# Kernel optimization log

Measured on AMD Instinct MI355X. Metric: run time of the kernel, lower is better.

Reference implementation:

```python
import jax, jax.numpy as jnp
import numpy as np

N = 1024      # total nodes in batch
H = 128       # node_dim == hid_dim
B = 128       # number of graphs
NPG = 8       # nodes per graph (<= MAX_NODES=9)
MAXN = 9
BT = 3        # bond_types
A = 3 * MAXN * MAXN  # action_space_length = 243


def setup_inputs() -> dict:
    key = jax.random.key(0)
    ks = jax.random.split(key, 8)
    node_features = jax.random.normal(ks[0], (N, H), jnp.float32) * 0.5
    seg = np.repeat(np.arange(B), NPG)  # contiguous graph membership (dgl batching)
    segment_ids = jnp.asarray(seg, jnp.int32)
    # len_vec[g, n] = 1 if node n belongs to graph g  ->  len_vec.T @ len_vec is the block-diagonal pair mask
    len_vec = jnp.asarray((seg[None, :] == np.arange(B)[:, None]).astype(np.float32))
    mask = jnp.zeros((B, A), jnp.float32)  # additive logit mask
    rng = np.random.default_rng(0)
    indexmask = jnp.asarray(np.argsort(rng.random((B, A)), axis=1).astype(np.int32))  # per-graph permutation of [0,243)
    batch_num_nodes = jnp.full((B,), NPG, jnp.int32)
    sc = lambda k, sh, fan: jax.random.normal(k, sh, jnp.float32) / np.sqrt(fan)
    W_fcv1 = sc(ks[1], (H, H // 2), H); b_fcv1 = jnp.zeros((H // 2,), jnp.float32)
    W_fcv2 = sc(ks[2], (H // 2, 1), H // 2); b_fcv2 = jnp.zeros((1,), jnp.float32)
    W_a2 = sc(ks[3], (2 * H, H), 2 * H); b_a2 = jnp.zeros((H,), jnp.float32)
    W_final = sc(ks[4], (H, BT), H); b_final = jnp.zeros((BT,), jnp.float32)
    return dict(node_features=node_features, len_vec=len_vec, mask=mask,
                W_fcv1=W_fcv1, b_fcv1=b_fcv1, W_fcv2=W_fcv2, b_fcv2=b_fcv2,
                W_a2=W_a2, b_a2=b_a2, W_final=W_final, b_final=b_final,
                indexmask=indexmask, segment_ids=segment_ids,
                batch_num_nodes=batch_num_nodes)


def reference(node_features, len_vec, mask, W_fcv1, b_fcv1, W_fcv2, b_fcv2,
              W_a2, b_a2, W_final, b_final, indexmask, segment_ids,
              batch_num_nodes):
    # --- value head: sum-pool per graph, relu(fcv1), fcv2 ---
    readout = jax.ops.segment_sum(node_features, segment_ids, num_segments=B)  # [B,H]
    readout = jax.nn.relu(readout @ W_fcv1 + b_fcv1) @ W_fcv2 + b_fcv2          # [B,1]

    # --- all-pairs features: cat([nf[i], nf[j]]) -> relu -> action_2 -> relu -> final ---
    # relu(cat(a,b)) = cat(relu(a),relu(b)); split W_a2 so we never materialize [N,N,2H]
    r = jax.nn.relu(node_features)          # [N,H]
    Ai = r @ W_a2[:H]                        # row-node (Y2) contribution  [N,H]
    Bj = r @ W_a2[H:]                        # col-node (X2) contribution  [N,H]
    hidden = jax.nn.relu(Ai[:, None, :] + Bj[None, :, :] + b_a2)   # [N,N,H]
    len_matrix = (len_vec.T @ len_vec)[..., None]                  # [N,N,1] block-diagonal 0/1
    scores = (jnp.einsum('ijh,hk->ijk', hidden, W_final) + b_final) * len_matrix  # [N,N,3]
    flat = scores.reshape(-1)

    # --- ragged per-graph gather of the nonzero (in-block) entries, padded to A=243 ---
    val = batch_num_nodes.astype(jnp.int32)          # [B]
    off = jnp.cumsum(val) - val                      # exclusive prefix (node offsets)
    s = jnp.arange(A, dtype=jnp.int32)[None, :]      # [1,A] slot index
    v = val[:, None]; o = off[:, None]
    i_loc = s // (v * BT)
    j_loc = (s % (v * BT)) // BT
    k = s % BT
    valid = s < v * v * BT                           # slots beyond val*val*3 are padding (-1 in torch code)
    flat_idx = ((o + i_loc) * N + (o + j_loc)) * BT + k
    flat_idx = jnp.clip(flat_idx, 0, N * N * BT - 1)
    gathered = jnp.where(valid, flat[flat_idx], jnp.float32(0.0))  # [B,A]

    # torch.index_select(final[idx], 0, indexmask[idx])
    fap = jnp.take_along_axis(gathered, indexmask.astype(jnp.int32), axis=1)
    probs = jax.nn.softmax(fap + mask, axis=1)
    return probs, readout
```

## Files before the change

### kernel.cpp

```cpp
#include <hip/hip_runtime.h>
#include <cfloat>

#define HH 128
#define BB 128
#define AA 243
#define MAXV 9

__device__ __forceinline__ float rl(float x, int l) {
    return __builtin_bit_cast(float, __builtin_amdgcn_readlane(__builtin_bit_cast(int, x), l));
}

__global__ __launch_bounds__(512) void apm_fused(
    const float* __restrict__ nf,
    const float* __restrict__ maskp,
    const float* __restrict__ W_fcv1,
    const float* __restrict__ b_fcv1,
    const float* __restrict__ W_fcv2,
    const float* __restrict__ b_fcv2,
    const float* __restrict__ W_a2,
    const float* __restrict__ b_a2,
    const float* __restrict__ W_final,
    const float* __restrict__ b_final,
    const int*   __restrict__ indexmask,
    const int*   __restrict__ bnn,
    float* __restrict__ probs_out,
    float* __restrict__ readout_out)
{
    const int b    = blockIdx.x;
    const int t    = threadIdx.x;
    const int lane = t & 63;
    const int w    = t >> 6;
    const int matB = w >> 2;
    const int hq   = w & 3;
    const int c0   = lane << 1;

    __shared__ float pS[2][4][MAXV][132];
    __shared__ float wfT[3][HH];
    __shared__ float sc[AA + 1];
    __shared__ float rdbuf[HH];
    __shared__ float rout[64];
    __shared__ float xred[16];

    int ov = 0;
    if (lane < b)      ov += bnn[lane];
    if (lane + 64 < b) ov += bnn[lane + 64];
    const int v = bnn[b];

    const float* Wb = W_a2 + matB * (HH * HH) + (hq * 32) * HH + c0;
    float2 wreg[32];
    #pragma unroll
    for (int h = 0; h < 32; ++h) wreg[h] = *(const float2*)(Wb + h * HH);

    float mk = 0.f, bfin = 0.f; int im = 0;
    if (t < AA) {
        im   = indexmask[b * AA + t];
        mk   = maskp[b * AA + t];
        bfin = b_final[t % 3];
    }
    if (t < 3 * HH) {
        int h = t / 3, k = t - 3 * h;
        wfT[k][h] = W_final[t];
    }

    #pragma unroll
    for (int o = 1; o < 64; o <<= 1) ov += __shfl_xor(ov, o, 64);
    const int off = ov;

    const int hbase = hq * 32 + (lane & 31);
    float rr[MAXV]; float rdsum = 0.f;
    #pragma unroll
    for (int i = 0; i < MAXV; ++i) {
        float x = (i < v) ? nf[(off + i) * HH + hbase] : 0.f;
        rdsum += x;
        rr[i]  = fmaxf(x, 0.f);
    }
    if (w < 4 && lane < 32) rdbuf[hbase] = rdsum;

    float accx[MAXV], accy[MAXV];
    #pragma unroll
    for (int i = 0; i < MAXV; ++i) { accx[i] = 0.f; accy[i] = 0.f; }
    #pragma unroll
    for (int h = 0; h < 32; ++h) {
        const float wx = wreg[h].x, wy = wreg[h].y;
        #pragma unroll
        for (int i = 0; i < MAXV; ++i) {
            const float s = rl(rr[i], h);
            accx[i] = fmaf(s, wx, accx[i]);
            accy[i] = fmaf(s, wy, accy[i]);
        }
    }
    #pragma unroll
    for (int i = 0; i < MAXV; ++i)
        *(float2*)&pS[matB][hq][i][c0] = make_float2(accx[i], accy[i]);
    __syncthreads();

    const int vv3 = v * v * 3;
    if (t < AA && t >= vv3) sc[t] = 0.f;

    float a2lo = 0.f;
    if (w < 6) {
        #pragma unroll
        for (int rep = 0; rep < 3; ++rep) {
            int idx = t + rep * 384;
            int m   = idx / 576;
            int rem = idx - m * 576;
            int i   = rem >> 6;
            int cc  = (rem & 63) << 1;
            float2 p0 = *(const float2*)&pS[m][0][i][cc];
            float2 p1 = *(const float2*)&pS[m][1][i][cc];
            float2 p2 = *(const float2*)&pS[m][2][i][cc];
            float2 p3 = *(const float2*)&pS[m][3][i][cc];
            float sx = (p0.x + p1.x) + (p2.x + p3.x);
            float sy = (p0.y + p1.y) + (p2.y + p3.y);
            if (m == 0) { sx += b_a2[cc]; sy += b_a2[cc + 1]; }
            *(float2*)&pS[m][0][i][cc] = make_float2(sx, sy);
        }
    } else if (w == 6) {
        float rd1 = rdbuf[64 + lane];
        float q0 = 0.f, q1 = 0.f, q2 = 0.f, q3 = 0.f;
        #pragma unroll
        for (int h = 0; h < 16; ++h) {
            q0 = fmaf(rl(rd1, h),      W_fcv1[(64 + h)  * 64 + lane], q0);
            q1 = fmaf(rl(rd1, h + 16), W_fcv1[(80 + h)  * 64 + lane], q1);
            q2 = fmaf(rl(rd1, h + 32), W_fcv1[(96 + h)  * 64 + lane], q2);
            q3 = fmaf(rl(rd1, h + 48), W_fcv1[(112 + h) * 64 + lane], q3);
        }
        rout[lane] = (q0 + q1) + (q2 + q3);
    } else {
        float rd0 = rdbuf[lane];
        float q0 = b_fcv1[lane], q1 = 0.f, q2 = 0.f, q3 = 0.f;
        #pragma unroll
        for (int h = 0; h < 16; ++h) {
            q0 = fmaf(rl(rd0, h),      W_fcv1[h        * 64 + lane], q0);
            q1 = fmaf(rl(rd0, h + 16), W_fcv1[(16 + h) * 64 + lane], q1);
            q2 = fmaf(rl(rd0, h + 32), W_fcv1[(32 + h) * 64 + lane], q2);
            q3 = fmaf(rl(rd0, h + 48), W_fcv1[(48 + h) * 64 + lane], q3);
        }
        a2lo = (q0 + q1) + (q2 + q3);
    }
    __syncthreads();

    if (t < vv3) {
        const int pair = t / 3, k = t - 3 * pair;
        const int i = pair / v, j = pair - i * v;
        const float* ar = &pS[0][0][i][0];
        const float* br = &pS[1][0][j][0];
        const float* wk = &wfT[k][0];
        float s0 = 0.f, s1 = 0.f, s2 = 0.f, s3 = 0.f;
        #pragma unroll 8
        for (int h = 0; h < HH; h += 4) {
            float4 a4 = *(const float4*)(ar + h);
            float4 b4 = *(const float4*)(br + h);
            float4 w4 = *(const float4*)(wk + h);
            s0 = fmaf(fmaxf(a4.x + b4.x, 0.f), w4.x, s0);
            s1 = fmaf(fmaxf(a4.y + b4.y, 0.f), w4.y, s1);
            s2 = fmaf(fmaxf(a4.z + b4.z, 0.f), w4.z, s2);
            s3 = fmaf(fmaxf(a4.w + b4.w, 0.f), w4.w, s3);
        }
        sc[t] = bfin + ((s0 + s1) + (s2 + s3));
    } else if (w == 7) {
        float a2 = a2lo + rout[lane];
        float x = fmaxf(a2, 0.f) * W_fcv2[lane];
        #pragma unroll
        for (int o = 1; o < 64; o <<= 1) x += __shfl_xor(x, o, 64);
        if (lane == 0) readout_out[b] = x + b_fcv2[0];
    }
    __syncthreads();

    float x = -FLT_MAX;
    if (t < AA) x = sc[im] + mk;
    float m = x;
    #pragma unroll
    for (int o = 1; o < 64; o <<= 1) m = fmaxf(m, __shfl_xor(m, o, 64));
    if (lane == 0) xred[w] = m;
    __syncthreads();
    m = fmaxf(fmaxf(xred[0], xred[1]), fmaxf(xred[2], xred[3]));
    float e = (t < AA) ? __expf(x - m) : 0.f;
    float s = e;
    #pragma unroll
    for (int o = 1; o < 64; o <<= 1) s += __shfl_xor(s, o, 64);
    if (lane == 0) xred[8 + w] = s;
    __syncthreads();
    const float denom = (xred[8] + xred[9]) + (xred[10] + xred[11]);
    const float rden  = __builtin_amdgcn_rcpf(denom);
    if (t < AA) probs_out[b * AA + t] = e * rden;
}

extern "C" void kernel_launch(void* const* d_in, const int* in_sizes, int n_in,
                              void* d_out, int out_size, void* d_ws, size_t ws_size,
                              hipStream_t stream) {
    const float* nf      = (const float*)d_in[0];
    const float* maskp   = (const float*)d_in[2];
    const float* W_fcv1  = (const float*)d_in[3];
    const float* b_fcv1  = (const float*)d_in[4];
    const float* W_fcv2  = (const float*)d_in[5];
    const float* b_fcv2  = (const float*)d_in[6];
    const float* W_a2    = (const float*)d_in[7];
    const float* b_a2    = (const float*)d_in[8];
    const float* W_final = (const float*)d_in[9];
    const float* b_final = (const float*)d_in[10];
    const int*   indexmask = (const int*)d_in[11];
    const int*   bnn       = (const int*)d_in[13];

    float* probs   = (float*)d_out;
    float* readout = probs + BB * AA;

    apm_fused<<<BB, 512, 0, stream>>>(nf, maskp, W_fcv1, b_fcv1, W_fcv2, b_fcv2,
                                      W_a2, b_a2, W_final, b_final,
                                      indexmask, bnn, probs, readout);
}
```

Before: 13.90 us.

## Use packed FMA GEMV, specialize for 8-node graphs, single-pass online softmax

Rewrites the per-block projection GEMV to issue v_pk_fma_f32 with two scalar-broadcast node values packed per instruction, halving FMA instruction count. Adds a template specialization for v==8 that drops the per-row predication and the 9th row of work. Replaces the two-barrier softmax reduction with per-wave max/sum pairs combined via exp rescaling, removing one __syncthreads. Inline asm and the extra exps add complexity, and the v==8 fast path is tied to the common graph size.

```diff
diff --git a/kernel.cpp b/kernel.cpp
--- a/kernel.cpp
+++ b/kernel.cpp
@@ -6,8 +6,57 @@
 #define AA 243
 #define MAXV 9
 
+typedef float v2f __attribute__((ext_vector_type(2)));
+
+__device__ __forceinline__ int rli(float x, int l) {
+    return __builtin_amdgcn_readlane(__builtin_bit_cast(int, x), l);
+}
 __device__ __forceinline__ float rl(float x, int l) {
     return __builtin_bit_cast(float, __builtin_amdgcn_readlane(__builtin_bit_cast(int, x), l));
+}
+__device__ __forceinline__ unsigned long long pack2(int lo, int hi) {
+    int2 p; p.x = lo; p.y = hi;
+    return __builtin_bit_cast(unsigned long long, p);
+}
+__device__ __forceinline__ void pk_fma_lo(v2f& acc, unsigned long long sv, v2f w) {
+    asm("v_pk_fma_f32 %0, %2, %1, %0 op_sel:[0,0,0] op_sel_hi:[0,1,1]"
+        : "+v"(acc) : "v"(w), "s"(sv));
+}
+__device__ __forceinline__ void pk_fma_hi(v2f& acc, unsigned long long sv, v2f w) {
+    asm("v_pk_fma_f32 %0, %2, %1, %0 op_sel:[1,0,0] op_sel_hi:[1,1,1]"
+        : "+v"(acc) : "v"(w), "s"(sv));
+}
+
+template<int NV, bool PRED>
+__device__ __forceinline__ void gemv_phase(
+    const float* __restrict__ nf, int off, int v, int hbase,
+    bool write_rd, float* __restrict__ rdbuf,
+    const v2f* __restrict__ wreg, float* __restrict__ dst, int c0)
+{
+    float rr[NV]; float rdsum = 0.f;
+    #pragma unroll
+    for (int i = 0; i < NV; ++i) {
+        float x = PRED ? ((i < v) ? nf[(off + i) * HH + hbase] : 0.f)
+                       : nf[(off + i) * HH + hbase];
+        rdsum += x;
+        rr[i] = fmaxf(x, 0.f);
+    }
+    if (write_rd) rdbuf[hbase] = rdsum;
+    v2f acc[NV];
+    #pragma unroll
+    for (int i = 0; i < NV; ++i) acc[i] = (v2f)(0.0f);
+    #pragma unroll
+    for (int h = 0; h < 32; h += 2) {
+        const v2f w0 = wreg[h], w1 = wreg[h + 1];
+        #pragma unroll
+        for (int i = 0; i < NV; ++i) {
+            unsigned long long sv = pack2(rli(rr[i], h), rli(rr[i], h + 1));
+            pk_fma_lo(acc[i], sv, w0);
+            pk_fma_hi(acc[i], sv, w1);
+        }
+    }
+    #pragma unroll
+    for (int i = 0; i < NV; ++i) *(v2f*)(dst + i * 132 + c0) = acc[i];
 }
 
 __global__ __launch_bounds__(512) void apm_fused(
@@ -39,7 +88,7 @@
     __shared__ float sc[AA + 1];
     __shared__ float rdbuf[HH];
     __shared__ float rout[64];
-    __shared__ float xred[16];
+    __shared__ float2 xr2[8];
 
     int ov = 0;
     if (lane < b)      ov += bnn[lane];
@@ -47,9 +96,9 @@
     const int v = bnn[b];
 
     const float* Wb = W_a2 + matB * (HH * HH) + (hq * 32) * HH + c0;
-    float2 wreg[32];
-    #pragma unroll
-    for (int h = 0; h < 32; ++h) wreg[h] = *(const float2*)(Wb + h * HH);
+    v2f wreg[32];
+    #pragma unroll
+    for (int h = 0; h < 32; ++h) wreg[h] = *(const v2f*)(Wb + h * HH);
 
     float mk = 0.f, bfin = 0.f; int im = 0;
     if (t < AA) {
@@ -66,36 +115,15 @@
     for (int o = 1; o < 64; o <<= 1) ov += __shfl_xor(ov, o, 64);
     const int off = ov;
 
-    const int hbase = hq * 32 + (lane & 31);
-    float rr[MAXV]; float rdsum = 0.f;
-    #pragma unroll
-    for (int i = 0; i < MAXV; ++i) {
-        float x = (i < v) ? nf[(off + i) * HH + hbase] : 0.f;
-        rdsum += x;
-        rr[i]  = fmaxf(x, 0.f);
-    }
-    if (w < 4 && lane < 32) rdbuf[hbase] = rdsum;
-
-    float accx[MAXV], accy[MAXV];
-    #pragma unroll
-    for (int i = 0; i < MAXV; ++i) { accx[i] = 0.f; accy[i] = 0.f; }
-    #pragma unroll
-    for (int h = 0; h < 32; ++h) {
-        const float wx = wreg[h].x, wy = wreg[h].y;
-        #pragma unroll
-        for (int i = 0; i < MAXV; ++i) {
-            const float s = rl(rr[i], h);
-            accx[i] = fmaf(s, wx, accx[i]);
-            accy[i] = fmaf(s, wy, accy[i]);
-        }
-    }
-    #pragma unroll
-    for (int i = 0; i < MAXV; ++i)
-        *(float2*)&pS[matB][hq][i][c0] = make_float2(accx[i], accy[i]);
-    __syncthreads();
-
     const int vv3 = v * v * 3;
     if (t < AA && t >= vv3) sc[t] = 0.f;
+
+    const int hbase = hq * 32 + (lane & 31);
+    const bool wrd  = (w < 4) && (lane < 32);
+    float* dst = &pS[matB][hq][0][0];
+    if (v == 8) gemv_phase<8, false>(nf, off, v, hbase, wrd, rdbuf, wreg, dst, c0);
+    else        gemv_phase<MAXV, true>(nf, off, v, hbase, wrd, rdbuf, wreg, dst, c0);
+    __syncthreads();
 
     float a2lo = 0.f;
     if (w < 6) {
@@ -169,21 +197,23 @@
 
     float x = -FLT_MAX;
     if (t < AA) x = sc[im] + mk;
-    float m = x;
-    #pragma unroll
-    for (int o = 1; o < 64; o <<= 1) m = fmaxf(m, __shfl_xor(m, o, 64));
-    if (lane == 0) xred[w] = m;
-    __syncthreads();
-    m = fmaxf(fmaxf(xred[0], xred[1]), fmaxf(xred[2], xred[3]));
-    float e = (t < AA) ? __expf(x - m) : 0.f;
-    float s = e;
-    #pragma unroll
-    for (int o = 1; o < 64; o <<= 1) s += __shfl_xor(s, o, 64);
-    if (lane == 0) xred[8 + w] = s;
-    __syncthreads();
-    const float denom = (xred[8] + xred[9]) + (xred[10] + xred[11]);
-    const float rden  = __builtin_amdgcn_rcpf(denom);
-    if (t < AA) probs_out[b * AA + t] = e * rden;
+    float m_w = x;
+    #pragma unroll
+    for (int o = 1; o < 64; o <<= 1) m_w = fmaxf(m_w, __shfl_xor(m_w, o, 64));
+    float e = (t < AA) ? __expf(x - m_w) : 0.f;
+    float s_w = e;
+    #pragma unroll
+    for (int o = 1; o < 64; o <<= 1) s_w += __shfl_xor(s_w, o, 64);
+    if (lane == 0 && w < 4) xr2[w] = make_float2(m_w, s_w);
+    __syncthreads();
+    if (t < AA) {
+        float2 p0 = xr2[0], p1 = xr2[1], p2 = xr2[2], p3 = xr2[3];
+        float m = fmaxf(fmaxf(p0.x, p1.x), fmaxf(p2.x, p3.x));
+        float denom = p0.y * __expf(p0.x - m) + p1.y * __expf(p1.x - m)
+                    + p2.y * __expf(p2.x - m) + p3.y * __expf(p3.x - m);
+        float f = __expf(m_w - m);
+        probs_out[b * AA + t] = e * f * __builtin_amdgcn_rcpf(denom);
+    }
 }
 
 extern "C" void kernel_launch(void* const* d_in, const int* in_sizes, int n_in,
```

New measurement: 13.52 us. 2.8% less time.
